# Performance work log

Hardware: AMD Instinct MI355X
Metric: run time of the kernel (lower is better)

## Reference

```python
import jax, jax.numpy as jnp
import numpy as np

BS, C, H, W = 64, 3, 512, 512
DROP_PIX = 0.3          # fraction of pixels dropped
NOISE_STD = 0.1         # gaussian multiplicative noise std
RNG_SEED = 42           # internal forward randomness (torch RNG analog)


def setup_inputs() -> dict:
    key = jax.random.key(0)
    x = jax.random.normal(key, (BS, C, H, W), dtype=jnp.float32)
    return {"x": x}


def reference(x):
    bs, c, h, w = x.shape
    hw = h * w
    len_keep = int(hw * (1.0 - DROP_PIX))
    k_mask, k_noise = jax.random.split(jax.random.key(RNG_SEED))

    # Per-sample random permutation of pixel indices, keep first len_keep.
    # argsort of iid uniforms == uniformly random permutation (all bs at once,
    # replacing the Python loop + per-iteration randperm of the original).
    u = jax.random.uniform(k_mask, (bs, hw))
    keep_idx = jnp.argsort(u, axis=1)[:, :len_keep]          # [bs, len_keep]
    mask = jnp.zeros((bs, hw), dtype=x.dtype)
    mask = mask.at[jnp.arange(bs)[:, None], keep_idx].set(1.0)
    mask = mask.reshape(bs, 1, h, w)

    # drop_type == 'zeros'
    x = x * mask

    # additive_noise: gaussian multiplicative noise (real-valued branch)
    noise = jax.random.normal(k_noise, x.shape, dtype=x.dtype) * NOISE_STD + 1.0
    x = x * noise
    return x, mask
```

## Files before the change

kernel.cpp:

```cpp
#include <hip/hip_runtime.h>

typedef unsigned int u32;
typedef unsigned long long u64;
typedef unsigned char u8;

__host__ __device__ __forceinline__ void tf2x32(u32 k0, u32 k1, u32 x0, u32 x1,
                                                u32& o0, u32& o1)
{
    const u32 ks2 = k0 ^ k1 ^ 0x1BD11BDAu;
    x0 += k0; x1 += k1;
#define TF_R(r) { x0 += x1; x1 = (x1 << (r)) | (x1 >> (32 - (r))); x1 ^= x0; }
    TF_R(13) TF_R(15) TF_R(26) TF_R(6)
    x0 += k1; x1 += ks2 + 1u;
    TF_R(17) TF_R(29) TF_R(16) TF_R(24)
    x0 += ks2; x1 += k0 + 2u;
    TF_R(13) TF_R(15) TF_R(26) TF_R(6)
    x0 += k0; x1 += k1 + 3u;
    TF_R(17) TF_R(29) TF_R(16) TF_R(24)
    x0 += k1; x1 += ks2 + 4u;
    TF_R(13) TF_R(15) TF_R(26) TF_R(6)
    x0 += ks2; x1 += k0 + 5u;
#undef TF_R
    o0 = x0; o1 = x1;
}

__device__ __forceinline__ u32 rbits(u32 k0, u32 k1, u32 e)
{
    u32 o0, o1; tf2x32(k0, k1, 0u, e, o0, o1); return o0 ^ o1;
}

#define HW        262144u
#define PMASK     262143u
#define KEEP      183500u
#define NX        50331648u
#define NM        16777216u
#define LO_F      (-0.99999994039535522461f)

#define WLO       5806464u
#define WWIDTH    131072u
#define NBIN      4096
#define ROWCAP    6144
#define BLKCAP    512

#define CAND_B    (64u * ROWCAP * 8u)
#define WS_BYTES  (CAND_B + 512u + 512u)

__device__ u64 g_cand[64 * ROWCAP];
__device__ u64 g_rowsel[64];
__device__ u32 g_cnts[128];

__device__ __forceinline__ float noise_from_bits(u32 bits)
{
    float f  = __uint_as_float((bits >> 9) | 0x3F800000u) - 1.0f;
    float un = fmaf(f, 2.0f, LO_F);
    un = fmaxf(LO_F, un);
    float w = -__logf(fmaf(-un, un, 1.0f));
    float p;
    if (w < 5.0f) {
        w -= 2.5f;
        p = 2.81022636e-08f;
        p = fmaf(p, w, 3.43273939e-07f);
        p = fmaf(p, w, -3.5233877e-06f);
        p = fmaf(p, w, -4.39150654e-06f);
        p = fmaf(p, w, 0.00021858087f);
        p = fmaf(p, w, -0.00125372503f);
        p = fmaf(p, w, -0.00417768164f);
        p = fmaf(p, w, 0.246640727f);
        p = fmaf(p, w, 1.50140941f);
    } else {
        w = __fsqrt_rn(w) - 3.0f;
        p = -0.000200214257f;
        p = fmaf(p, w, 0.000100950558f);
        p = fmaf(p, w, 0.00134934322f);
        p = fmaf(p, w, -0.00367342844f);
        p = fmaf(p, w, 0.00573950773f);
        p = fmaf(p, w, -0.0076224613f);
        p = fmaf(p, w, 0.00943887047f);
        p = fmaf(p, w, 1.00167406f);
        p = fmaf(p, w, 2.83297682f);
    }
    float ei = p * un;
    return fmaf(1.41421356f * ei, 0.1f, 1.0f);
}

__global__ __launch_bounds__(256) void k1_scan(u32 mk0, u32 mk1,
                                               u32* __restrict__ cnts,
                                               u64* __restrict__ cand)
{
    __shared__ u64 s_cand[BLKCAP];
    __shared__ u32 s_cnt, s_below, s_base;
    const int t = threadIdx.x;
    const u32 blk = blockIdx.x;
    const u32 row = blk >> 4;
    const u32 base = blk << 14;
    if (t == 0) { s_cnt = 0; s_below = 0; }
    __syncthreads();
    u32 below = 0;
#pragma unroll 1
    for (int i = 0; i < 16; ++i) {
        u32 vi = (u32)(i << 8) + (u32)t;
        u32 e = base + (vi << 2);
#pragma unroll
        for (int j = 0; j < 4; ++j) {
            u32 m = rbits(mk0, mk1, e + (u32)j) >> 9;
            below += (m < WLO) ? 1u : 0u;
            if (m - WLO < WWIDTH) {
                u32 p = ((blk & 15u) << 14) + (vi << 2) + (u32)j;
                u32 pos = atomicAdd(&s_cnt, 1u);
                if (pos < BLKCAP) s_cand[pos] = ((u64)m << 18) | (u64)p;
            }
        }
    }
    atomicAdd(&s_below, below);
    __syncthreads();
    u32 cnt = s_cnt; if (cnt > BLKCAP) cnt = BLKCAP;
    if (t == 0) {
        atomicAdd(&cnts[row], s_below);
        s_base = atomicAdd(&cnts[64 + row], cnt);
    }
    __syncthreads();
    u32 gbase = s_base;
    for (u32 i = (u32)t; i < cnt; i += 256u) {
        u32 gi = gbase + i;
        if (gi < ROWCAP) cand[row * ROWCAP + gi] = s_cand[i];
    }
}

__global__ __launch_bounds__(256) void k2_select(u32* __restrict__ cnts,
                                                 const u64* __restrict__ cand,
                                                 u64* __restrict__ rowsel)
{
    __shared__ u32 h[NBIN];
    __shared__ u32 sh[258];
    __shared__ u64 tie[64];
    __shared__ u32 tiecnt;
    const int t = threadIdx.x;
    const u32 row = blockIdx.x;
    u32 n = cnts[64 + row]; if (n > ROWCAP) n = ROWCAP;
    u32 below = cnts[row];
    u32 r = KEEP - below;
#pragma unroll
    for (int i = 0; i < NBIN / 256; ++i) h[t + (i << 8)] = 0;
    if (t == 0) tiecnt = 0;
    __syncthreads();
    const u64* rc = cand + row * ROWCAP;
    for (u32 i = (u32)t; i < n; i += 256u) {
        u32 m = (u32)(rc[i] >> 18);
        atomicAdd(&h[(m - WLO) >> 5], 1u);
    }
    __syncthreads();
    u32 v[16]; u32 s = 0;
#pragma unroll
    for (int i = 0; i < 16; ++i) { v[i] = h[t * 16 + i]; s += v[i]; }
    sh[t] = s;
    __syncthreads();
    if (t == 0) {
        u32 run = 0; u32 c = 0;
        for (; c < 255u; ++c) { u32 cs = sh[c]; if (run + cs >= r) break; run += cs; }
        sh[256] = c; sh[257] = run;
    }
    __syncthreads();
    u32 c = sh[256];
    if (t == (int)c) {
        u32 run = sh[257];
        u32 b = (u32)t * 16u + 15u; u32 r2 = r - run;
#pragma unroll
        for (int i = 0; i < 16; ++i) {
            if (run + v[i] >= r) { b = (u32)t * 16u + (u32)i; r2 = r - run; break; }
            run += v[i];
        }
        sh[256] = b; sh[257] = r2;
    }
    __syncthreads();
    u32 bstar = sh[256], r2 = sh[257];
    u32 mlo = WLO + (bstar << 5), mhi = mlo + 32u;
    for (u32 i = (u32)t; i < n; i += 256u) {
        u64 k = rc[i];
        u32 m = (u32)(k >> 18);
        if (m >= mlo && m < mhi) {
            u32 pos = atomicAdd(&tiecnt, 1u);
            if (pos < 64u) tie[pos] = k;
        }
    }
    __syncthreads();
    if (t == 0) {
        u32 cnt = tiecnt; if (cnt > 64u) cnt = 64u;
        if (r2 > cnt) r2 = cnt;
        u64 kst = 0;
        for (u32 it = 0; it < r2; ++it) {
            u64 mn = ~0ull; u32 mi = 0;
            for (u32 i2 = 0; i2 < cnt; ++i2) if (tie[i2] < mn) { mn = tie[i2]; mi = i2; }
            kst = mn; tie[mi] = ~0ull;
        }
        rowsel[row] = kst;
        cnts[row] = 0;
        cnts[64 + row] = 0;
    }
}

__global__ __launch_bounds__(256) void k34_final(const float4* __restrict__ x4,
                                                 float4* __restrict__ out4,
                                                 float4* __restrict__ mask4,
                                                 const u64* __restrict__ rowsel,
                                                 u32 mk0, u32 mk1, u32 nk0, u32 nk1)
{
    u32 tid = blockIdx.x * 256u + threadIdx.x;
    u32 row = tid >> 16;
    u64 kst = rowsel[row];
    u32 e = tid << 2;
    u32 p = e & PMASK;

    u32 m0 = rbits(mk0, mk1, e)      >> 9;
    u32 m1 = rbits(mk0, mk1, e + 1u) >> 9;
    u32 m2 = rbits(mk0, mk1, e + 2u) >> 9;
    u32 m3 = rbits(mk0, mk1, e + 3u) >> 9;
    float4 mk;
    mk.x = ((((u64)m0 << 18) | (u64)(p))      <= kst) ? 1.0f : 0.0f;
    mk.y = ((((u64)m1 << 18) | (u64)(p + 1u)) <= kst) ? 1.0f : 0.0f;
    mk.z = ((((u64)m2 << 18) | (u64)(p + 2u)) <= kst) ? 1.0f : 0.0f;
    mk.w = ((((u64)m3 << 18) | (u64)(p + 3u)) <= kst) ? 1.0f : 0.0f;
    mask4[tid] = mk;

    u32 b3 = row * 3u;
#pragma unroll
    for (u32 cc = 0; cc < 3u; ++cc) {
        u32 en = ((b3 + cc) << 18) | p;
        float4 xv = x4[en >> 2];
        float4 r;
        r.x = (xv.x * mk.x) * noise_from_bits(rbits(nk0, nk1, en));
        r.y = (xv.y * mk.y) * noise_from_bits(rbits(nk0, nk1, en + 1u));
        r.z = (xv.z * mk.z) * noise_from_bits(rbits(nk0, nk1, en + 2u));
        r.w = (xv.w * mk.w) * noise_from_bits(rbits(nk0, nk1, en + 3u));
        out4[en >> 2] = r;
    }
}

extern "C" void kernel_launch(void* const* d_in, const int* in_sizes, int n_in,
                              void* d_out, int out_size, void* d_ws, size_t ws_size,
                              hipStream_t stream) {
    const float* x = (const float*)d_in[0];
    float* xout = (float*)d_out;
    float* maskf = xout + NX;

    u32 mk0, mk1, nk0, nk1;
    tf2x32(0u, 42u, 0u, 0u, mk0, mk1);
    tf2x32(0u, 42u, 0u, 1u, nk0, nk1);

    u64* cand; u64* rowsel; u32* cnts;
    if (d_ws != nullptr && ws_size >= (size_t)WS_BYTES) {
        u8* w = (u8*)d_ws;
        cand   = (u64*)w;
        rowsel = (u64*)(w + CAND_B);
        cnts   = (u32*)(w + CAND_B + 512u);
        hipMemsetAsync(cnts, 0, 512u, stream);
    } else {
        hipGetSymbolAddress((void**)&cand,   HIP_SYMBOL(g_cand));
        hipGetSymbolAddress((void**)&rowsel, HIP_SYMBOL(g_rowsel));
        hipGetSymbolAddress((void**)&cnts,   HIP_SYMBOL(g_cnts));
    }

    k1_scan<<<1024, 256, 0, stream>>>(mk0, mk1, cnts, cand);
    k2_select<<<64, 256, 0, stream>>>(cnts, cand, rowsel);
    k34_final<<<16384, 256, 0, stream>>>((const float4*)x, (float4*)xout,
                                         (float4*)maskf, rowsel,
                                         mk0, mk1, nk0, nk1);
    (void)in_sizes; (void)n_in; (void)out_size;
}
```

Before: 493.3 us.

## Materialize keep-mask bitmap in scan/select to skip threefry recompute in final pass

The scan kernel now records a 1-bit-per-pixel bitmap of pixels definitely below the selection window using wavefront ballots. The select kernel ORs in the in-window candidates that fall at or below the threshold key. The final kernel then reads this bitmap instead of regenerating four threefry hashes per thread to rebuild the mask. This removes one of the two Philox-style RNG evaluations per pixel in the heavy pass, at the cost of a 2MB bitmap write and read plus global atomics. The counters move to a device global, and the per-call memset is removed; the select kernel resets them at its end.

```diff
diff --git a/kernel.cpp b/kernel.cpp
--- a/kernel.cpp
+++ b/kernel.cpp
@@ -34,6 +34,7 @@
 #define KEEP      183500u
 #define NX        50331648u
 #define NM        16777216u
+#define NWORD     524288u
 #define LO_F      (-0.99999994039535522461f)
 
 #define WLO       5806464u
@@ -42,11 +43,12 @@
 #define ROWCAP    6144
 #define BLKCAP    512
 
+#define BITM_B    (NWORD * 4u)
 #define CAND_B    (64u * ROWCAP * 8u)
-#define WS_BYTES  (CAND_B + 512u + 512u)
-
+#define WS_BYTES  (BITM_B + CAND_B)
+
+__device__ u32 g_bitm[NWORD];
 __device__ u64 g_cand[64 * ROWCAP];
-__device__ u64 g_rowsel[64];
 __device__ u32 g_cnts[128];
 
 __device__ __forceinline__ float noise_from_bits(u32 bits)
@@ -84,12 +86,14 @@
 }
 
 __global__ __launch_bounds__(256) void k1_scan(u32 mk0, u32 mk1,
-                                               u32* __restrict__ cnts,
+                                               u32* __restrict__ bitm,
                                                u64* __restrict__ cand)
 {
     __shared__ u64 s_cand[BLKCAP];
     __shared__ u32 s_cnt, s_below, s_base;
     const int t = threadIdx.x;
+    const u32 l = (u32)t & 63u;
+    const u32 w = (u32)t >> 6;
     const u32 blk = blockIdx.x;
     const u32 row = blk >> 4;
     const u32 base = blk << 14;
@@ -98,25 +102,34 @@
     u32 below = 0;
 #pragma unroll 1
     for (int i = 0; i < 16; ++i) {
-        u32 vi = (u32)(i << 8) + (u32)t;
-        u32 e = base + (vi << 2);
+        const u32 base0 = base + ((u32)i << 10) + (w << 8);
+        u64 bal[4];
 #pragma unroll
         for (int j = 0; j < 4; ++j) {
-            u32 m = rbits(mk0, mk1, e + (u32)j) >> 9;
-            below += (m < WLO) ? 1u : 0u;
-            if (m - WLO < WWIDTH) {
-                u32 p = ((blk & 15u) << 14) + (vi << 2) + (u32)j;
+            u32 e = base0 + ((u32)j << 6) + l;
+            u32 m = rbits(mk0, mk1, e) >> 9;
+            u32 d = m - WLO;
+            below += d >> 31;
+            bal[j] = __ballot((int)(d >> 31));
+            if (d < WWIDTH) {
                 u32 pos = atomicAdd(&s_cnt, 1u);
-                if (pos < BLKCAP) s_cand[pos] = ((u64)m << 18) | (u64)p;
+                if (pos < BLKCAP) s_cand[pos] = ((u64)m << 18) | (u64)(e & PMASK);
             }
         }
+        if (l < 8u) {
+            u32 qi = l >> 1;
+            u64 b = (qi == 0u) ? bal[0] : (qi == 1u) ? bal[1]
+                  : (qi == 2u) ? bal[2] : bal[3];
+            u32 wv = (l & 1u) ? (u32)(b >> 32) : (u32)b;
+            bitm[(base0 >> 5) + l] = wv;
+        }
     }
     atomicAdd(&s_below, below);
     __syncthreads();
     u32 cnt = s_cnt; if (cnt > BLKCAP) cnt = BLKCAP;
     if (t == 0) {
-        atomicAdd(&cnts[row], s_below);
-        s_base = atomicAdd(&cnts[64 + row], cnt);
+        atomicAdd(&g_cnts[row], s_below);
+        s_base = atomicAdd(&g_cnts[64 + row], cnt);
     }
     __syncthreads();
     u32 gbase = s_base;
@@ -126,18 +139,18 @@
     }
 }
 
-__global__ __launch_bounds__(256) void k2_select(u32* __restrict__ cnts,
-                                                 const u64* __restrict__ cand,
-                                                 u64* __restrict__ rowsel)
+__global__ __launch_bounds__(256) void k2_select(const u64* __restrict__ cand,
+                                                 u32* __restrict__ bitm)
 {
     __shared__ u32 h[NBIN];
     __shared__ u32 sh[258];
     __shared__ u64 tie[64];
     __shared__ u32 tiecnt;
+    __shared__ u64 s_kst;
     const int t = threadIdx.x;
     const u32 row = blockIdx.x;
-    u32 n = cnts[64 + row]; if (n > ROWCAP) n = ROWCAP;
-    u32 below = cnts[row];
+    u32 n = g_cnts[64 + row]; if (n > ROWCAP) n = ROWCAP;
+    u32 below = g_cnts[row];
     u32 r = KEEP - below;
 #pragma unroll
     for (int i = 0; i < NBIN / 256; ++i) h[t + (i << 8)] = 0;
@@ -192,35 +205,41 @@
             for (u32 i2 = 0; i2 < cnt; ++i2) if (tie[i2] < mn) { mn = tie[i2]; mi = i2; }
             kst = mn; tie[mi] = ~0ull;
         }
-        rowsel[row] = kst;
-        cnts[row] = 0;
-        cnts[64 + row] = 0;
+        s_kst = kst;
+    }
+    __syncthreads();
+    u64 kst = s_kst;
+    for (u32 i = (u32)t; i < n; i += 256u) {
+        u64 k = rc[i];
+        if (k <= kst) {
+            u32 p = (u32)k & PMASK;
+            atomicOr(&bitm[(row << 13) + (p >> 5)], 1u << (p & 31u));
+        }
+    }
+    if (t == 0) {
+        g_cnts[row] = 0;
+        g_cnts[64 + row] = 0;
     }
 }
 
 __global__ __launch_bounds__(256) void k34_final(const float4* __restrict__ x4,
                                                  float4* __restrict__ out4,
                                                  float4* __restrict__ mask4,
-                                                 const u64* __restrict__ rowsel,
-                                                 u32 mk0, u32 mk1, u32 nk0, u32 nk1)
+                                                 const u32* __restrict__ bitm,
+                                                 u32 nk0, u32 nk1)
 {
     u32 tid = blockIdx.x * 256u + threadIdx.x;
+    u32 wrd = bitm[tid >> 3];
+    u32 nib = wrd >> ((tid & 7u) << 2);
+    float4 mk;
+    mk.x = (nib & 1u) ? 1.0f : 0.0f;
+    mk.y = (nib & 2u) ? 1.0f : 0.0f;
+    mk.z = (nib & 4u) ? 1.0f : 0.0f;
+    mk.w = (nib & 8u) ? 1.0f : 0.0f;
+    mask4[tid] = mk;
+
     u32 row = tid >> 16;
-    u64 kst = rowsel[row];
-    u32 e = tid << 2;
-    u32 p = e & PMASK;
-
-    u32 m0 = rbits(mk0, mk1, e)      >> 9;
-    u32 m1 = rbits(mk0, mk1, e + 1u) >> 9;
-    u32 m2 = rbits(mk0, mk1, e + 2u) >> 9;
-    u32 m3 = rbits(mk0, mk1, e + 3u) >> 9;
-    float4 mk;
-    mk.x = ((((u64)m0 << 18) | (u64)(p))      <= kst) ? 1.0f : 0.0f;
-    mk.y = ((((u64)m1 << 18) | (u64)(p + 1u)) <= kst) ? 1.0f : 0.0f;
-    mk.z = ((((u64)m2 << 18) | (u64)(p + 2u)) <= kst) ? 1.0f : 0.0f;
-    mk.w = ((((u64)m3 << 18) | (u64)(p + 3u)) <= kst) ? 1.0f : 0.0f;
-    mask4[tid] = mk;
-
+    u32 p = (tid << 2) & PMASK;
     u32 b3 = row * 3u;
 #pragma unroll
     for (u32 cc = 0; cc < 3u; ++cc) {
@@ -246,23 +265,19 @@
     tf2x32(0u, 42u, 0u, 0u, mk0, mk1);
     tf2x32(0u, 42u, 0u, 1u, nk0, nk1);
 
-    u64* cand; u64* rowsel; u32* cnts;
+    u32* bitm; u64* cand;
     if (d_ws != nullptr && ws_size >= (size_t)WS_BYTES) {
-        u8* w = (u8*)d_ws;
-        cand   = (u64*)w;
-        rowsel = (u64*)(w + CAND_B);
-        cnts   = (u32*)(w + CAND_B + 512u);
-        hipMemsetAsync(cnts, 0, 512u, stream);
+        u8* wsp = (u8*)d_ws;
+        bitm = (u32*)wsp;
+        cand = (u64*)(wsp + BITM_B);
     } else {
-        hipGetSymbolAddress((void**)&cand,   HIP_SYMBOL(g_cand));
-        hipGetSymbolAddress((void**)&rowsel, HIP_SYMBOL(g_rowsel));
-        hipGetSymbolAddress((void**)&cnts,   HIP_SYMBOL(g_cnts));
-    }
-
-    k1_scan<<<1024, 256, 0, stream>>>(mk0, mk1, cnts, cand);
-    k2_select<<<64, 256, 0, stream>>>(cnts, cand, rowsel);
+        hipGetSymbolAddress((void**)&bitm, HIP_SYMBOL(g_bitm));
+        hipGetSymbolAddress((void**)&cand, HIP_SYMBOL(g_cand));
+    }
+
+    k1_scan<<<1024, 256, 0, stream>>>(mk0, mk1, bitm, cand);
+    k2_select<<<64, 256, 0, stream>>>(cand, bitm);
     k34_final<<<16384, 256, 0, stream>>>((const float4*)x, (float4*)xout,
-                                         (float4*)maskf, rowsel,
-                                         mk0, mk1, nk0, nk1);
+                                         (float4*)maskf, bitm, nk0, nk1);
     (void)in_sizes; (void)n_in; (void)out_size;
 }
```

Result: faster. 475.1 us, median of 2 (-3.7%).
